# Kernel optimization log

Hardware: AMD Instinct MI355X
Metric: run time of the kernel (lower is better)

## Reference

```python
import jax, jax.numpy as jnp
import numpy as np

B, NZ, L = 8, 16, 512
E, DM, NH, HD = 256, 512, 16, 32
FF, NL, E1D, PDIM, PMAX = 1024, 8, 32, 64, 24
EPS_LN = 1e-5
EPS_D = 1e-12


def _ln(x, g, b):
    m = jnp.mean(x, axis=-1, keepdims=True)
    v = jnp.mean((x - m) ** 2, axis=-1, keepdims=True)
    return (x - m) / jnp.sqrt(v + EPS_LN) * g + b


def setup_inputs() -> dict:
    key = jax.random.key(0)
    ks = iter(jax.random.split(key, 32))
    rn = lambda shape, fan: jax.random.normal(next(ks), shape, jnp.float32) / np.float32(np.sqrt(fan))
    inp = {
        "z": jax.random.normal(next(ks), (B, NZ, L), jnp.float32),
        "x": jax.random.uniform(next(ks), (B, 20, L), jnp.float32),
        # embeddings
        "pos_table": rn((2 * PMAX + 1, PDIM), 1.0),
        "aa_table": rn((20, E1D), 1.0),
        # embed_x: Linear(nz,E), relu, Linear(E,E)
        "ex_w1": rn((NZ, E), NZ), "ex_b1": jnp.zeros((E,), jnp.float32),
        "ex_w2": rn((E, E), E), "ex_b2": jnp.zeros((E,), jnp.float32),
        # per-layer stacked params
        "Wq": rn((NL, E, DM), E), "Wk": rn((NL, E, DM), E), "Wv": rn((NL, E, DM), E),
        "Wo": rn((NL, DM, E), DM), "bo": jnp.zeros((NL, E), jnp.float32),
        "W2d": rn((NL, PDIM, NH), PDIM), "b2d": jnp.zeros((NL, NH), jnp.float32),
        "W1": rn((NL, E + E1D, FF), E + E1D), "b1": jnp.zeros((NL, FF), jnp.float32),
        "W2": rn((NL, FF, E), FF), "b2": jnp.zeros((NL, E), jnp.float32),
        "g1": jnp.ones((NL, E), jnp.float32), "be1": jnp.zeros((NL, E), jnp.float32),
        "g2": jnp.ones((NL, E), jnp.float32), "be2": jnp.zeros((NL, E), jnp.float32),
        # mlp_3d: Linear(E,E), relu, Linear(E,3)
        "m3_w1": rn((E, E), E), "m3_b1": jnp.zeros((E,), jnp.float32),
        "m3_w2": rn((E, 3), E), "m3_b2": jnp.zeros((3,), jnp.float32),
    }
    return inp


def reference(z, x, pos_table, aa_table, ex_w1, ex_b1, ex_w2, ex_b2,
              Wq, Wk, Wv, Wo, bo, W2d, b2d, W1, b1, W2, b2,
              g1, be1, g2, be2, m3_w1, m3_b1, m3_w2, m3_b2):
    Bn, _, Ln = z.shape
    h = jnp.transpose(z, (0, 2, 1))  # (B, L, nz)
    # relative-position bins: argmin over integer bins == clip to [-PMAX, PMAX]
    rel = jnp.arange(Ln)[None, :] - jnp.arange(Ln)[:, None]
    bins = jnp.clip(rel, -PMAX, PMAX) + PMAX
    pe = pos_table[bins]  # (L, L, PDIM), batch-replicated
    e_aa = aa_table[jnp.argmax(x, axis=1)]  # (B, L, E1D)
    # embed_x MLP
    h = jax.nn.relu(h @ ex_w1 + ex_b1) @ ex_w2 + ex_b2  # (B, L, E)
    scale = np.float32(1.0 / np.sqrt(DM))  # dp_attn_norm='d_model'
    for i in range(NL):
        q = (h @ Wq[i]).reshape(Bn, Ln, NH, HD) * scale
        k = (h @ Wk[i]).reshape(Bn, Ln, NH, HD)
        v = (h @ Wv[i]).reshape(Bn, Ln, NH, HD)
        # learned pairwise bias: mlp_2d then transpose(1,3).transpose(2,3) -> bias[h,i,j] = out[i,j,h]
        bias = jnp.einsum('lmp,ph->hlm', pe, W2d[i]) + b2d[i][:, None, None]
        scores = jnp.einsum('blhd,bmhd->bhlm', q, k) + bias[None]
        attn = jax.nn.softmax(scores, axis=-1)
        o = jnp.einsum('bhlm,bmhd->blhd', attn, v).reshape(Bn, Ln, DM)
        h = _ln(h + (o @ Wo[i] + bo[i]), g1[i], be1[i])
        um = jnp.concatenate([h, e_aa], axis=-1)  # (B, L, E+E1D)
        s2 = jax.nn.relu(um @ W1[i] + b1[i]) @ W2[i] + b2[i]
        h = _ln(h + s2, g2[i], be2[i])
    r = jax.nn.relu(h @ m3_w1 + m3_b1) @ m3_w2 + m3_b2  # (B, L, 3)
    # distance map (get_coords=False path)
    d = jnp.sqrt(jnp.sum((r[:, None, :, :] - r[:, :, None, :]) ** 2, axis=-1) + EPS_D)
    return d  # (B, L, L)
```

## Files before the change

kernel.cpp:

```cpp
#include <hip/hip_runtime.h>
#include <math.h>

constexpr int Bn = 8, NZ = 16, Ln = 512;
constexpr int E = 256, DM = 512, NH = 16, HD = 32;
constexpr int FF = 1024, NL = 8, E1D = 32, PDIM = 64, PMAX = 24;
constexpr int ROWS = Bn * Ln;
constexpr float QSCALE = 0.04419417382415922f;

typedef __attribute__((ext_vector_type(8))) short bf16x8;
typedef __attribute__((ext_vector_type(4))) float floatx4;

__device__ inline unsigned short f2b(float f) {
  union { float f; unsigned u; } v; v.f = f;
  unsigned r = (v.u + 0x7FFF + ((v.u >> 16) & 1)) >> 16;
  return (unsigned short)r;
}
__device__ inline float b2f(unsigned short u) {
  union { unsigned u; float f; } v; v.u = ((unsigned)u) << 16; return v.f;
}

__device__ inline void gll16(const void* g, void* l) {
  __builtin_amdgcn_global_load_lds(
      (const __attribute__((address_space(1))) void*)g,
      (__attribute__((address_space(3))) void*)l, 16, 0, 0);
}

__global__ __launch_bounds__(256) void transpose_qkv(
    const float* __restrict__ Wq, const float* __restrict__ Wk,
    const float* __restrict__ Wv, unsigned short* __restrict__ qkvT)
{
  __shared__ float t[32][33];
  int zb = blockIdx.z;
  int which = zb / NL, l = zb % NL;
  const float* s = (which == 0 ? Wq : which == 1 ? Wk : Wv) + (size_t)l * E * DM;
  unsigned short* d = qkvT + (size_t)l * 3 * DM * E + (size_t)which * DM * E;
  int c0 = blockIdx.x * 32, r0 = blockIdx.y * 32;
  int tx = threadIdx.x & 31, ty = threadIdx.x >> 5;
  #pragma unroll
  for (int i = 0; i < 4; ++i)
    t[ty + i * 8][tx] = s[(size_t)(r0 + ty + i * 8) * DM + c0 + tx];
  __syncthreads();
  #pragma unroll
  for (int i = 0; i < 4; ++i)
    d[(size_t)(c0 + ty + i * 8) * E + r0 + tx] = f2b(t[tx][ty + i * 8]);
}

__global__ __launch_bounds__(256) void transpose_bf16(
    const float* __restrict__ src, unsigned short* __restrict__ dst,
    int R, int C, size_t sls, size_t dls)
{
  __shared__ float t[32][33];
  int l = blockIdx.z;
  int c0 = blockIdx.x * 32, r0 = blockIdx.y * 32;
  int tx = threadIdx.x & 31, ty = threadIdx.x >> 5;
  const float* s = src + (size_t)l * sls;
  unsigned short* d = dst + (size_t)l * dls;
  #pragma unroll
  for (int i = 0; i < 4; ++i)
    t[ty + i * 8][tx] = s[(size_t)(r0 + ty + i * 8) * C + c0 + tx];
  __syncthreads();
  #pragma unroll
  for (int i = 0; i < 4; ++i)
    d[(size_t)(c0 + ty + i * 8) * R + r0 + tx] = f2b(t[tx][ty + i * 8]);
}

__global__ __launch_bounds__(256) void embed1_kernel(
    const float* __restrict__ z, const float* __restrict__ x,
    const float* __restrict__ aa,
    const float* __restrict__ w1, const float* __restrict__ b1,
    float* __restrict__ t0, unsigned short* __restrict__ umb)
{
  int row = blockIdx.x;
  int b = row >> 9, l = row & (Ln - 1);
  int t = threadIdx.x;
  __shared__ float zs[NZ];
  __shared__ int am_s;
  if (t < NZ) zs[t] = z[((size_t)b * NZ + t) * Ln + l];
  if (t == 0) {
    const float* xp = x + (size_t)b * 20 * Ln + l;
    int am = 0; float bv = xp[0];
    for (int c = 1; c < 20; ++c) { float vv = xp[(size_t)c * Ln]; if (vv > bv) { bv = vv; am = c; } }
    am_s = am;
  }
  __syncthreads();
  float a1 = b1[t];
  #pragma unroll
  for (int nz = 0; nz < NZ; ++nz) a1 += zs[nz] * w1[nz * E + t];
  t0[(size_t)row * E + t] = fmaxf(a1, 0.f);
  if (t < E1D) umb[(size_t)row * (E + E1D) + E + t] = f2b(aa[am_s * E1D + t]);
}

__global__ __launch_bounds__(256) void bias_kernel(
    const float* __restrict__ pos, const float* __restrict__ W2d,
    const float* __restrict__ b2d, float* __restrict__ bias49)
{
  int layer = blockIdx.x;
  for (int idx = threadIdx.x; idx < NH * 49; idx += 256) {
    int hh = idx / 49, bin = idx % 49;
    float acc = b2d[layer * NH + hh];
    for (int p = 0; p < PDIM; ++p)
      acc += pos[bin * PDIM + p] * W2d[((size_t)layer * PDIM + p) * NH + hh];
    bias49[(size_t)layer * NH * 49 + hh * 49 + bin] = acc;
  }
}

template<int BM, int BN, int BK, bool BIAS, bool RELU, bool OUTBF16, bool QKV>
__global__ __launch_bounds__(256) void gemm_mfma(
    const unsigned short* __restrict__ A, const unsigned short* __restrict__ Bt,
    const float* __restrict__ bias,
    float* __restrict__ Cf, unsigned short* __restrict__ Cb, int N, int K)
{
  constexpr int MT = BM / 32, NT = BN / 32;
  __shared__ __align__(16) unsigned short As[BM][BK];
  __shared__ __align__(16) unsigned short Bs[BN][BK];
  const int tid = threadIdx.x;
  const int wave = tid >> 6, ln = tid & 63;
  const int quad = ln >> 4, l16 = ln & 15;
  const int wm = wave >> 1, wn = wave & 1;
  const int m0 = blockIdx.y * BM, n0 = blockIdx.x * BN;

  floatx4 acc[MT][NT] = {};

  if constexpr (BK == 32) {
    const int lrow = ln >> 2, chunk = ln & 3;
    const int schunk = chunk ^ ((lrow >> 1) & 3);
    const unsigned short* aSrc = A + (size_t)(m0 + wave * 16 + lrow) * K + schunk * 8;
    const unsigned short* bSrc = Bt + (size_t)(n0 + wave * 16 + lrow) * K + schunk * 8;
    const int rkey = (l16 >> 1) & 3;

    for (int kb = 0; kb < K; kb += 32) {
      __syncthreads();
      #pragma unroll
      for (int it = 0; it < BM / 64; ++it)
        gll16(aSrc + (size_t)it * 64 * K + kb, &As[it * 64 + wave * 16][0]);
      #pragma unroll
      for (int it = 0; it < BN / 64; ++it)
        gll16(bSrc + (size_t)it * 64 * K + kb, &Bs[it * 64 + wave * 16][0]);
      __syncthreads();
      bf16x8 af[MT], bfr[NT];
      #pragma unroll
      for (int i = 0; i < MT; ++i)
        af[i] = *(const bf16x8*)&As[wm * (BM / 2) + i * 16 + l16][(quad ^ rkey) * 8];
      #pragma unroll
      for (int j = 0; j < NT; ++j)
        bfr[j] = *(const bf16x8*)&Bs[wn * (BN / 2) + j * 16 + l16][(quad ^ rkey) * 8];
      #pragma unroll
      for (int i = 0; i < MT; ++i)
        #pragma unroll
        for (int j = 0; j < NT; ++j)
          acc[i][j] = __builtin_amdgcn_mfma_f32_16x16x32_bf16(af[i], bfr[j], acc[i][j], 0, 0, 0);
    }
  } else {
    const int lrow = ln >> 4, chunk = ln & 15;
    const int key = wave * 4 + lrow;
    const int schunk = chunk ^ key;
    const unsigned short* aSrc = A + (size_t)(m0 + key) * K + schunk * 8;
    const unsigned short* bSrc = Bt + (size_t)(n0 + key) * K + schunk * 8;

    for (int kb = 0; kb < K; kb += 128) {
      __syncthreads();
      #pragma unroll
      for (int it = 0; it < BM / 16; ++it)
        gll16(aSrc + (size_t)(it * 16) * K + kb, &As[it * 16 + wave * 4][0]);
      #pragma unroll
      for (int it = 0; it < BN / 16; ++it)
        gll16(bSrc + (size_t)(it * 16) * K + kb, &Bs[it * 16 + wave * 4][0]);
      __syncthreads();
      #pragma unroll
      for (int kc = 0; kc < 4; ++kc) {
        bf16x8 af[MT], bfr[NT];
        #pragma unroll
        for (int i = 0; i < MT; ++i)
          af[i] = *(const bf16x8*)&As[wm * (BM / 2) + i * 16 + l16][(((kc * 4 + quad) ^ l16) * 8)];
        #pragma unroll
        for (int j = 0; j < NT; ++j)
          bfr[j] = *(const bf16x8*)&Bs[wn * (BN / 2) + j * 16 + l16][(((kc * 4 + quad) ^ l16) * 8)];
        #pragma unroll
        for (int i = 0; i < MT; ++i)
          #pragma unroll
          for (int j = 0; j < NT; ++j)
            acc[i][j] = __builtin_amdgcn_mfma_f32_16x16x32_bf16(af[i], bfr[j], acc[i][j], 0, 0, 0);
      }
    }
  }

  #pragma unroll
  for (int i = 0; i < MT; ++i)
    #pragma unroll
    for (int j = 0; j < NT; ++j) {
      int col = n0 + wn * (BN / 2) + j * 16 + l16;
      float bv = BIAS ? bias[col] : 0.f;
      float sc = QKV ? (col < 512 ? QSCALE : 1.f) : 1.f;
      #pragma unroll
      for (int r = 0; r < 4; ++r) {
        int rowg = m0 + wm * (BM / 2) + i * 16 + quad * 4 + r;
        float v = acc[i][j][r] * sc + bv;
        if (RELU) v = fmaxf(v, 0.f);
        if (OUTBF16) Cb[(size_t)rowg * N + col] = f2b(v);
        else Cf[(size_t)rowg * N + col] = v;
      }
    }
}

__global__ __launch_bounds__(256) void gemm_ln(
    const unsigned short* __restrict__ A, const unsigned short* __restrict__ Bt,
    const float* __restrict__ bias, float* __restrict__ h,
    const float* __restrict__ g, const float* __restrict__ be,
    unsigned short* __restrict__ outb, int bstride, int K)
{
  __shared__ __align__(16) unsigned short As[16][128];
  __shared__ __align__(16) unsigned short Bs[256][128];
  __shared__ __align__(16) float vtile[16][260];
  const int tid = threadIdx.x;
  const int w = tid >> 6, ln = tid & 63;
  const int quad = ln >> 4, l16 = ln & 15;
  const int m0 = blockIdx.x * 16;
  const int lrow = ln >> 4, chunk = ln & 15;
  const int key = w * 4 + lrow;
  const int schunk = chunk ^ key;
  const unsigned short* aSrc = A + (size_t)(m0 + key) * K + schunk * 8;
  const unsigned short* bSrc = Bt + (size_t)key * K + schunk * 8;

  floatx4 acc[4] = {};

  for (int kb = 0; kb < K; kb += 128) {
    __syncthreads();
    gll16(aSrc + kb, &As[w * 4][0]);
    #pragma unroll
    for (int it = 0; it < 16; ++it)
      gll16(bSrc + (size_t)(it * 16) * K + kb, &Bs[it * 16 + w * 4][0]);
    __syncthreads();
    #pragma unroll
    for (int kc = 0; kc < 4; ++kc) {
      bf16x8 af = *(const bf16x8*)&As[l16][(((kc * 4 + quad) ^ l16) * 8)];
      #pragma unroll
      for (int nt = 0; nt < 4; ++nt) {
        bf16x8 bf = *(const bf16x8*)&Bs[w * 64 + nt * 16 + l16][(((kc * 4 + quad) ^ l16) * 8)];
        acc[nt] = __builtin_amdgcn_mfma_f32_16x16x32_bf16(af, bf, acc[nt], 0, 0, 0);
      }
    }
  }

  #pragma unroll
  for (int nt = 0; nt < 4; ++nt) {
    int col = w * 64 + nt * 16 + l16;
    float bv = bias[col];
    #pragma unroll
    for (int r = 0; r < 4; ++r) {
      int row = quad * 4 + r;
      vtile[row][col] = acc[nt][r] + bv + h[(size_t)(m0 + row) * E + col];
    }
  }
  __syncthreads();

  const int c0 = ln * 4;
  #pragma unroll
  for (int rr = 0; rr < 4; ++rr) {
    const int lr = w * 4 + rr;
    float4 v = *(const float4*)&vtile[lr][c0];
    float s = v.x + v.y + v.z + v.w;
    float s2 = v.x * v.x + v.y * v.y + v.z * v.z + v.w * v.w;
    #pragma unroll
    for (int off = 1; off < 64; off <<= 1) {
      s += __shfl_xor(s, off, 64);
      s2 += __shfl_xor(s2, off, 64);
    }
    const float mean = s * (1.f / E);
    const float rstd = rsqrtf(s2 * (1.f / E) - mean * mean + 1e-5f);
    const float4 gv = *(const float4*)(g + c0);
    const float4 bv = *(const float4*)(be + c0);
    float4 y;
    y.x = (v.x - mean) * rstd * gv.x + bv.x;
    y.y = (v.y - mean) * rstd * gv.y + bv.y;
    y.z = (v.z - mean) * rstd * gv.z + bv.z;
    y.w = (v.w - mean) * rstd * gv.w + bv.w;
    const size_t row = (size_t)(m0 + lr);
    *(float4*)(h + row * E + c0) = y;
    ushort4 yb;
    yb.x = f2b(y.x); yb.y = f2b(y.y); yb.z = f2b(y.z); yb.w = f2b(y.w);
    *(ushort4*)(outb + row * (size_t)bstride + c0) = yb;
  }
}

__global__ __launch_bounds__(256) void attn_kernel(
    const unsigned short* __restrict__ qkv, const float* __restrict__ bias49,
    unsigned short* __restrict__ o)
{
  const int i0 = blockIdx.x * 64;
  const int bh = blockIdx.y;
  const int b = bh >> 4, hh = bh & 15;
  const int tid = threadIdx.x;
  const int wave = tid >> 6, ln = tid & 63;
  const int quad = ln >> 4, l16 = ln & 15;

  __shared__ __align__(16) unsigned short Kt[64][40];
  __shared__ __align__(16) unsigned short Vt[32][72];
  __shared__ __align__(16) unsigned short Pw[4][2][16][72];
  __shared__ float bsh[49];

  if (tid < 49) bsh[tid] = bias49[hh * 49 + tid];

  const unsigned short* qkvb = qkv + (size_t)b * Ln * 1536;

  const int qrow = i0 + wave * 16 + l16;
  const bf16x8 qf = *(const bf16x8*)(qkvb + (size_t)qrow * 1536 + hh * 32 + quad * 8);

  float m[4], l[4];
  #pragma unroll
  for (int r = 0; r < 4; ++r) { m[r] = -1e30f; l[r] = 0.f; }
  floatx4 acc_o[2] = {};

  const int krow = tid >> 2, kch = (tid & 3) * 8;
  const int vkey = tid & 63, vch = (tid >> 6) * 8;

  for (int jt = 0; jt < 8; ++jt) {
    const int j0 = jt * 64;
    __syncthreads();
    *(float4*)&Kt[krow][kch] =
        *(const float4*)(qkvb + (size_t)(j0 + krow) * 1536 + 512 + hh * 32 + kch);
    bf16x8 vv = *(const bf16x8*)(qkvb + (size_t)(j0 + vkey) * 1536 + 1024 + hh * 32 + vch);
    #pragma unroll
    for (int i = 0; i < 8; ++i) Vt[vch + i][vkey] = (unsigned short)vv[i];
    __syncthreads();

    floatx4 s4[4];
    #pragma unroll
    for (int t = 0; t < 4; ++t) {
      bf16x8 kf = *(const bf16x8*)&Kt[16 * t + l16][quad * 8];
      s4[t] = __builtin_amdgcn_mfma_f32_16x16x32_bf16(qf, kf, (floatx4){0.f, 0.f, 0.f, 0.f}, 0, 0, 0);
    }
    const int relmin = j0 - (i0 + 63), relmax = j0 + 63 - i0;
    if (relmin >= PMAX) {
      float bc = bsh[48];
      #pragma unroll
      for (int t = 0; t < 4; ++t)
        #pragma unroll
        for (int r = 0; r < 4; ++r) s4[t][r] += bc;
    } else if (relmax <= -PMAX) {
      float bc = bsh[0];
      #pragma unroll
      for (int t = 0; t < 4; ++t)
        #pragma unroll
        for (int r = 0; r < 4; ++r) s4[t][r] += bc;
    } else {
      const int base_rel = (j0 + l16) - (i0 + wave * 16 + quad * 4);
      #pragma unroll
      for (int t = 0; t < 4; ++t)
        #pragma unroll
        for (int r = 0; r < 4; ++r) {
          int rel = base_rel + 16 * t - r;
          rel = rel < -PMAX ? -PMAX : (rel > PMAX ? PMAX : rel);
          s4[t][r] += bsh[rel + PMAX];
        }
    }

    float mloc[4], alpha[4], psum[4];
    #pragma unroll
    for (int r = 0; r < 4; ++r) {
      mloc[r] = fmaxf(fmaxf(s4[0][r], s4[1][r]), fmaxf(s4[2][r], s4[3][r]));
      #pragma unroll
      for (int off = 1; off < 16; off <<= 1)
        mloc[r] = fmaxf(mloc[r], __shfl_xor(mloc[r], off, 64));
      float mnew = fmaxf(m[r], mloc[r]);
      alpha[r] = __expf(m[r] - mnew);
      m[r] = mnew;
      psum[r] = 0.f;
    }
    #pragma unroll
    for (int t = 0; t < 4; ++t)
      #pragma unroll
      for (int r = 0; r < 4; ++r) {
        float p = __expf(s4[t][r] - m[r]);
        s4[t][r] = p;
        psum[r] += p;
      }
    #pragma unroll
    for (int r = 0; r < 4; ++r) {
      #pragma unroll
      for (int off = 1; off < 16; off <<= 1)
        psum[r] += __shfl_xor(psum[r], off, 64);
      l[r] = l[r] * alpha[r] + psum[r];
      acc_o[0][r] *= alpha[r];
      acc_o[1][r] *= alpha[r];
    }

    #pragma unroll
    for (int t = 0; t < 4; ++t)
      #pragma unroll
      for (int r = 0; r < 4; ++r) {
        float p = s4[t][r];
        unsigned short hi = f2b(p);
        unsigned short lo = f2b(p - b2f(hi));
        Pw[wave][0][quad * 4 + r][16 * t + l16] = hi;
        Pw[wave][1][quad * 4 + r][16 * t + l16] = lo;
      }

    #pragma unroll
    for (int kh = 0; kh < 2; ++kh) {
      bf16x8 phi = *(const bf16x8*)&Pw[wave][0][l16][kh * 32 + quad * 8];
      bf16x8 plo = *(const bf16x8*)&Pw[wave][1][l16][kh * 32 + quad * 8];
      #pragma unroll
      for (int nt = 0; nt < 2; ++nt) {
        bf16x8 vf = *(const bf16x8*)&Vt[nt * 16 + l16][kh * 32 + quad * 8];
        acc_o[nt] = __builtin_amdgcn_mfma_f32_16x16x32_bf16(phi, vf, acc_o[nt], 0, 0, 0);
        acc_o[nt] = __builtin_amdgcn_mfma_f32_16x16x32_bf16(plo, vf, acc_o[nt], 0, 0, 0);
      }
    }
  }

  #pragma unroll
  for (int r = 0; r < 4; ++r) {
    float inv = 1.f / l[r];
    size_t rowg = (size_t)b * Ln + i0 + wave * 16 + quad * 4 + r;
    #pragma unroll
    for (int nt = 0; nt < 2; ++nt)
      o[rowg * 512 + hh * 32 + nt * 16 + l16] = f2b(acc_o[nt][r] * inv);
  }
}

template<bool RELU, bool BIAS, bool MIRROR>
__global__ __launch_bounds__(256) void gemm64f(
    const float* __restrict__ A, const float* __restrict__ B,
    const float* __restrict__ bias, float* __restrict__ C,
    unsigned short* __restrict__ mir, int N, int K)
{
  __shared__ __align__(16) float As[16][64];
  __shared__ __align__(16) float Bss[16][68];
  const int tid = threadIdx.x;
  const int tx = tid & 15, ty = tid >> 4;
  const int m0 = blockIdx.y * 64, n0 = blockIdx.x * 64;
  const int arow = tid >> 2, acol = (tid & 3) * 4;
  const int brow = tid >> 6, bcol = tid & 63;
  float acc[4][4] = {};
  for (int kb = 0; kb < K; kb += 16) {
    __syncthreads();
    float4 av = *(const float4*)(A + (size_t)(m0 + arow) * K + kb + acol);
    As[acol + 0][arow] = av.x; As[acol + 1][arow] = av.y;
    As[acol + 2][arow] = av.z; As[acol + 3][arow] = av.w;
    #pragma unroll
    for (int kk = 0; kk < 4; ++kk)
      Bss[brow + kk * 4][bcol] = B[(size_t)(kb + brow + kk * 4) * N + n0 + bcol];
    __syncthreads();
    #pragma unroll
    for (int k = 0; k < 16; ++k) {
      float4 a = *(const float4*)&As[k][4 * ty];
      float4 b = *(const float4*)&Bss[k][4 * tx];
      float av4[4] = {a.x, a.y, a.z, a.w};
      float bv4[4] = {b.x, b.y, b.z, b.w};
      #pragma unroll
      for (int ii = 0; ii < 4; ++ii)
        #pragma unroll
        for (int jj = 0; jj < 4; ++jj)
          acc[ii][jj] += av4[ii] * bv4[jj];
    }
  }
  #pragma unroll
  for (int ii = 0; ii < 4; ++ii) {
    size_t row = (size_t)m0 + 4 * ty + ii;
    int col = n0 + 4 * tx;
    float4 vv;
    vv.x = acc[ii][0]; vv.y = acc[ii][1]; vv.z = acc[ii][2]; vv.w = acc[ii][3];
    if (BIAS) {
      float4 bb = *(const float4*)(bias + col);
      vv.x += bb.x; vv.y += bb.y; vv.z += bb.z; vv.w += bb.w;
    }
    if (RELU) {
      vv.x = fmaxf(vv.x, 0.f); vv.y = fmaxf(vv.y, 0.f);
      vv.z = fmaxf(vv.z, 0.f); vv.w = fmaxf(vv.w, 0.f);
    }
    *(float4*)(C + row * N + col) = vv;
    if (MIRROR) {
      ushort4 mv;
      mv.x = f2b(vv.x); mv.y = f2b(vv.y); mv.z = f2b(vv.z); mv.w = f2b(vv.w);
      *(ushort4*)(mir + row * N + col) = mv;
    }
  }
}

__global__ __launch_bounds__(256) void final_r_kernel(
    const float* __restrict__ t1, const float* __restrict__ w2,
    const float* __restrict__ b2, float* __restrict__ r)
{
  int row = blockIdx.x, t = threadIdx.x;
  float xv = t1[(size_t)row * E + t];
  float p0 = xv * w2[t * 3 + 0];
  float p1 = xv * w2[t * 3 + 1];
  float p2 = xv * w2[t * 3 + 2];
  #pragma unroll
  for (int off = 32; off > 0; off >>= 1) {
    p0 += __shfl_down(p0, off, 64);
    p1 += __shfl_down(p1, off, 64);
    p2 += __shfl_down(p2, off, 64);
  }
  __shared__ float red[4][3];
  if ((t & 63) == 0) { int w = t >> 6; red[w][0] = p0; red[w][1] = p1; red[w][2] = p2; }
  __syncthreads();
  if (t < 3)
    r[(size_t)row * 3 + t] = red[0][t] + red[1][t] + red[2][t] + red[3][t] + b2[t];
}

__global__ __launch_bounds__(512) void dist_kernel(
    const float* __restrict__ r, float* __restrict__ out)
{
  int bi = blockIdx.x;
  int j = threadIdx.x;
  int b = bi >> 9;
  float x0 = r[(size_t)bi * 3 + 0];
  float y0 = r[(size_t)bi * 3 + 1];
  float z0 = r[(size_t)bi * 3 + 2];
  const float* rj = r + ((size_t)b * Ln + j) * 3;
  float dx = rj[0] - x0, dy = rj[1] - y0, dz = rj[2] - z0;
  out[(size_t)bi * Ln + j] = sqrtf(dx * dx + dy * dy + dz * dz + 1e-12f);
}

extern "C" void kernel_launch(void* const* d_in, const int* in_sizes, int n_in,
                              void* d_out, int out_size, void* d_ws, size_t ws_size,
                              hipStream_t stream)
{
  const float* z     = (const float*)d_in[0];
  const float* x     = (const float*)d_in[1];
  const float* pos   = (const float*)d_in[2];
  const float* aa    = (const float*)d_in[3];
  const float* ex_w1 = (const float*)d_in[4];
  const float* ex_b1 = (const float*)d_in[5];
  const float* ex_w2 = (const float*)d_in[6];
  const float* ex_b2 = (const float*)d_in[7];
  const float* Wq    = (const float*)d_in[8];
  const float* Wk    = (const float*)d_in[9];
  const float* Wv    = (const float*)d_in[10];
  const float* Wo    = (const float*)d_in[11];
  const float* bo    = (const float*)d_in[12];
  const float* W2d   = (const float*)d_in[13];
  const float* b2d   = (const float*)d_in[14];
  const float* W1    = (const float*)d_in[15];
  const float* b1    = (const float*)d_in[16];
  const float* W2    = (const float*)d_in[17];
  const float* b2    = (const float*)d_in[18];
  const float* g1    = (const float*)d_in[19];
  const float* be1   = (const float*)d_in[20];
  const float* g2    = (const float*)d_in[21];
  const float* be2   = (const float*)d_in[22];
  const float* m3w1  = (const float*)d_in[23];
  const float* m3b1  = (const float*)d_in[24];
  const float* m3w2  = (const float*)d_in[25];
  const float* m3b2  = (const float*)d_in[26];

  float* ws     = (float*)d_ws;
  float* h      = ws;
  float* t0     = h + (size_t)ROWS * E;
  float* r      = t0 + (size_t)ROWS * E;
  float* bias49 = r + (size_t)ROWS * 3;
  unsigned short* us = (unsigned short*)(bias49 + NL * NH * 49);
  unsigned short* hb   = us;
  unsigned short* umb  = hb  + (size_t)ROWS * E;
  unsigned short* qkvb = umb + (size_t)ROWS * (E + E1D);
  unsigned short* ob   = qkvb + (size_t)ROWS * 3 * DM;
  unsigned short* t1b  = ob  + (size_t)ROWS * DM;
  unsigned short* qkvT = t1b + (size_t)ROWS * FF;
  unsigned short* WoT  = qkvT + (size_t)NL * 3 * DM * E;
  unsigned short* W1T  = WoT  + (size_t)NL * E * DM;
  unsigned short* W2T  = W1T  + (size_t)NL * FF * (E+E1D);
  float* t1f = (float*)t1b;

  transpose_qkv<<<dim3(DM/32, E/32, 3*NL), 256, 0, stream>>>(Wq, Wk, Wv, qkvT);
  transpose_bf16<<<dim3(E/32, DM/32, NL), 256, 0, stream>>>(
      Wo, WoT, DM, E, (size_t)DM * E, (size_t)DM * E);
  transpose_bf16<<<dim3(FF/32, (E+E1D)/32, NL), 256, 0, stream>>>(
      W1, W1T, E + E1D, FF, (size_t)(E+E1D) * FF, (size_t)(E+E1D) * FF);
  transpose_bf16<<<dim3(E/32, FF/32, NL), 256, 0, stream>>>(
      W2, W2T, FF, E, (size_t)FF * E, (size_t)FF * E);

  embed1_kernel<<<ROWS, 256, 0, stream>>>(z, x, aa, ex_w1, ex_b1, t0, umb);
  gemm64f<false,true,true><<<dim3(E/64, ROWS/64), 256, 0, stream>>>(
      t0, ex_w2, ex_b2, h, hb, E, E);
  bias_kernel<<<NL, 256, 0, stream>>>(pos, W2d, b2d, bias49);

  for (int i = 0; i < NL; ++i) {
    gemm_mfma<64,128,128,false,false,true,true><<<dim3(12, 64), 256, 0, stream>>>(
        hb, qkvT + (size_t)i * 3 * DM * E, nullptr, nullptr, qkvb, 3 * DM, E);
    attn_kernel<<<dim3(Ln/64, Bn*NH), 256, 0, stream>>>(
        qkvb, bias49 + (size_t)i * NH * 49, ob);
    gemm_ln<<<ROWS/16, 256, 0, stream>>>(
        ob, WoT + (size_t)i * DM * E, bo + (size_t)i * E, h,
        g1 + (size_t)i * E, be1 + (size_t)i * E, umb, E + E1D, DM);
    gemm_mfma<64,64,32,true,true,true,false><<<dim3(FF/64, ROWS/64), 256, 0, stream>>>(
        umb, W1T + (size_t)i * FF * (E+E1D), b1 + (size_t)i * FF, nullptr, t1b, FF, E + E1D);
    gemm_ln<<<ROWS/16, 256, 0, stream>>>(
        t1b, W2T + (size_t)i * E * FF, b2 + (size_t)i * E, h,
        g2 + (size_t)i * E, be2 + (size_t)i * E, hb, E, FF);
  }

  gemm64f<true,true,false><<<dim3(E/64, ROWS/64), 256, 0, stream>>>(
      h, m3w1, m3b1, t1f, nullptr, E, E);
  final_r_kernel<<<ROWS, 256, 0, stream>>>(t1f, m3w2, m3b2, r);
  dist_kernel<<<ROWS, 512, 0, stream>>>(r, (float*)d_out);
}
```

Before: 813.6 us.

## Double-buffer K/V tiles with register prefetch and process 128 queries per block

```diff
diff --git a/kernel.cpp b/kernel.cpp
--- a/kernel.cpp
+++ b/kernel.cpp
@@ -286,15 +286,15 @@
     const unsigned short* __restrict__ qkv, const float* __restrict__ bias49,
     unsigned short* __restrict__ o)
 {
-  const int i0 = blockIdx.x * 64;
+  const int i0 = blockIdx.x * 128;
   const int bh = blockIdx.y;
   const int b = bh >> 4, hh = bh & 15;
   const int tid = threadIdx.x;
   const int wave = tid >> 6, ln = tid & 63;
   const int quad = ln >> 4, l16 = ln & 15;
 
-  __shared__ __align__(16) unsigned short Kt[64][40];
-  __shared__ __align__(16) unsigned short Vt[32][72];
+  __shared__ __align__(16) unsigned short Kt[2][64][40];
+  __shared__ __align__(16) unsigned short Vt[2][32][72];
   __shared__ __align__(16) unsigned short Pw[4][2][16][72];
   __shared__ float bsh[49];
 
@@ -302,120 +302,140 @@
 
   const unsigned short* qkvb = qkv + (size_t)b * Ln * 1536;
 
-  const int qrow = i0 + wave * 16 + l16;
-  const bf16x8 qf = *(const bf16x8*)(qkvb + (size_t)qrow * 1536 + hh * 32 + quad * 8);
-
-  float m[4], l[4];
-  #pragma unroll
-  for (int r = 0; r < 4; ++r) { m[r] = -1e30f; l[r] = 0.f; }
-  floatx4 acc_o[2] = {};
+  bf16x8 qf[2];
+  #pragma unroll
+  for (int u = 0; u < 2; ++u) {
+    const int qrow = i0 + wave * 32 + u * 16 + l16;
+    qf[u] = *(const bf16x8*)(qkvb + (size_t)qrow * 1536 + hh * 32 + quad * 8);
+  }
+
+  float m[2][4], l[2][4];
+  #pragma unroll
+  for (int u = 0; u < 2; ++u)
+    #pragma unroll
+    for (int r = 0; r < 4; ++r) { m[u][r] = -1e30f; l[u][r] = 0.f; }
+  floatx4 acc_o[2][2] = {};
 
   const int krow = tid >> 2, kch = (tid & 3) * 8;
   const int vkey = tid & 63, vch = (tid >> 6) * 8;
+  const unsigned short* kp = qkvb + (size_t)krow * 1536 + 512 + hh * 32 + kch;
+  const unsigned short* vp = qkvb + (size_t)vkey * 1536 + 1024 + hh * 32 + vch;
+
+  float4 kreg = *(const float4*)kp;
+  bf16x8 vreg = *(const bf16x8*)vp;
 
   for (int jt = 0; jt < 8; ++jt) {
     const int j0 = jt * 64;
+    const int cur = jt & 1;
+    *(float4*)&Kt[cur][krow][kch] = kreg;
+    #pragma unroll
+    for (int i = 0; i < 8; ++i) Vt[cur][vch + i][vkey] = (unsigned short)vreg[i];
     __syncthreads();
-    *(float4*)&Kt[krow][kch] =
-        *(const float4*)(qkvb + (size_t)(j0 + krow) * 1536 + 512 + hh * 32 + kch);
-    bf16x8 vv = *(const bf16x8*)(qkvb + (size_t)(j0 + vkey) * 1536 + 1024 + hh * 32 + vch);
-    #pragma unroll
-    for (int i = 0; i < 8; ++i) Vt[vch + i][vkey] = (unsigned short)vv[i];
-    __syncthreads();
-
-    floatx4 s4[4];
-    #pragma unroll
-    for (int t = 0; t < 4; ++t) {
-      bf16x8 kf = *(const bf16x8*)&Kt[16 * t + l16][quad * 8];
-      s4[t] = __builtin_amdgcn_mfma_f32_16x16x32_bf16(qf, kf, (floatx4){0.f, 0.f, 0.f, 0.f}, 0, 0, 0);
-    }
-    const int relmin = j0 - (i0 + 63), relmax = j0 + 63 - i0;
-    if (relmin >= PMAX) {
-      float bc = bsh[48];
+    if (jt < 7) {
+      kreg = *(const float4*)(kp + (size_t)(j0 + 64) * 1536);
+      vreg = *(const bf16x8*)(vp + (size_t)(j0 + 64) * 1536);
+    }
+
+    #pragma unroll
+    for (int u = 0; u < 2; ++u) {
+      const int qbase = i0 + wave * 32 + u * 16;
+
+      floatx4 s4[4];
+      #pragma unroll
+      for (int t = 0; t < 4; ++t) {
+        bf16x8 kf = *(const bf16x8*)&Kt[cur][16 * t + l16][quad * 8];
+        s4[t] = __builtin_amdgcn_mfma_f32_16x16x32_bf16(qf[u], kf, (floatx4){0.f, 0.f, 0.f, 0.f}, 0, 0, 0);
+      }
+      const int relmin = j0 - (qbase + 15), relmax = j0 + 63 - qbase;
+      if (relmin >= PMAX) {
+        float bc = bsh[48];
+        #pragma unroll
+        for (int t = 0; t < 4; ++t)
+          #pragma unroll
+          for (int r = 0; r < 4; ++r) s4[t][r] += bc;
+      } else if (relmax <= -PMAX) {
+        float bc = bsh[0];
+        #pragma unroll
+        for (int t = 0; t < 4; ++t)
+          #pragma unroll
+          for (int r = 0; r < 4; ++r) s4[t][r] += bc;
+      } else {
+        const int base_rel = (j0 + l16) - (qbase + quad * 4);
+        #pragma unroll
+        for (int t = 0; t < 4; ++t)
+          #pragma unroll
+          for (int r = 0; r < 4; ++r) {
+            int rel = base_rel + 16 * t - r;
+            rel = rel < -PMAX ? -PMAX : (rel > PMAX ? PMAX : rel);
+            s4[t][r] += bsh[rel + PMAX];
+          }
+      }
+
+      float mloc[4], alpha[4], psum[4];
+      #pragma unroll
+      for (int r = 0; r < 4; ++r) {
+        mloc[r] = fmaxf(fmaxf(s4[0][r], s4[1][r]), fmaxf(s4[2][r], s4[3][r]));
+        #pragma unroll
+        for (int off = 1; off < 16; off <<= 1)
+          mloc[r] = fmaxf(mloc[r], __shfl_xor(mloc[r], off, 64));
+        float mnew = fmaxf(m[u][r], mloc[r]);
+        alpha[r] = __expf(m[u][r] - mnew);
+        m[u][r] = mnew;
+        psum[r] = 0.f;
+      }
       #pragma unroll
       for (int t = 0; t < 4; ++t)
         #pragma unroll
-        for (int r = 0; r < 4; ++r) s4[t][r] += bc;
-    } else if (relmax <= -PMAX) {
-      float bc = bsh[0];
+        for (int r = 0; r < 4; ++r) {
+          float p = __expf(s4[t][r] - m[u][r]);
+          s4[t][r] = p;
+          psum[r] += p;
+        }
+      #pragma unroll
+      for (int r = 0; r < 4; ++r) {
+        #pragma unroll
+        for (int off = 1; off < 16; off <<= 1)
+          psum[r] += __shfl_xor(psum[r], off, 64);
+        l[u][r] = l[u][r] * alpha[r] + psum[r];
+        acc_o[u][0][r] *= alpha[r];
+        acc_o[u][1][r] *= alpha[r];
+      }
+
       #pragma unroll
       for (int t = 0; t < 4; ++t)
         #pragma unroll
-        for (int r = 0; r < 4; ++r) s4[t][r] += bc;
-    } else {
-      const int base_rel = (j0 + l16) - (i0 + wave * 16 + quad * 4);
-      #pragma unroll
-      for (int t = 0; t < 4; ++t)
-        #pragma unroll
         for (int r = 0; r < 4; ++r) {
-          int rel = base_rel + 16 * t - r;
-          rel = rel < -PMAX ? -PMAX : (rel > PMAX ? PMAX : rel);
-          s4[t][r] += bsh[rel + PMAX];
+          float p = s4[t][r];
+          unsigned short hi = f2b(p);
+          unsigned short lo = f2b(p - b2f(hi));
+          Pw[wave][0][quad * 4 + r][16 * t + l16] = hi;
+          Pw[wave][1][quad * 4 + r][16 * t + l16] = lo;
         }
-    }
-
-    float mloc[4], alpha[4], psum[4];
+
+      #pragma unroll
+      for (int kh = 0; kh < 2; ++kh) {
+        bf16x8 phi = *(const bf16x8*)&Pw[wave][0][l16][kh * 32 + quad * 8];
+        bf16x8 plo = *(const bf16x8*)&Pw[wave][1][l16][kh * 32 + quad * 8];
+        #pragma unroll
+        for (int nt = 0; nt < 2; ++nt) {
+          bf16x8 vf = *(const bf16x8*)&Vt[cur][nt * 16 + l16][kh * 32 + quad * 8];
+          acc_o[u][nt] = __builtin_amdgcn_mfma_f32_16x16x32_bf16(phi, vf, acc_o[u][nt], 0, 0, 0);
+          acc_o[u][nt] = __builtin_amdgcn_mfma_f32_16x16x32_bf16(plo, vf, acc_o[u][nt], 0, 0, 0);
+        }
+      }
+    }
+  }
+
+  #pragma unroll
+  for (int u = 0; u < 2; ++u)
     #pragma unroll
     for (int r = 0; r < 4; ++r) {
-      mloc[r] = fmaxf(fmaxf(s4[0][r], s4[1][r]), fmaxf(s4[2][r], s4[3][r]));
-      #pragma unroll
-      for (int off = 1; off < 16; off <<= 1)
-        mloc[r] = fmaxf(mloc[r], __shfl_xor(mloc[r], off, 64));
-      float mnew = fmaxf(m[r], mloc[r]);
-      alpha[r] = __expf(m[r] - mnew);
-      m[r] = mnew;
-      psum[r] = 0.f;
-    }
-    #pragma unroll
-    for (int t = 0; t < 4; ++t)
-      #pragma unroll
-      for (int r = 0; r < 4; ++r) {
-        float p = __expf(s4[t][r] - m[r]);
-        s4[t][r] = p;
-        psum[r] += p;
-      }
-    #pragma unroll
-    for (int r = 0; r < 4; ++r) {
-      #pragma unroll
-      for (int off = 1; off < 16; off <<= 1)
-        psum[r] += __shfl_xor(psum[r], off, 64);
-      l[r] = l[r] * alpha[r] + psum[r];
-      acc_o[0][r] *= alpha[r];
-      acc_o[1][r] *= alpha[r];
-    }
-
-    #pragma unroll
-    for (int t = 0; t < 4; ++t)
-      #pragma unroll
-      for (int r = 0; r < 4; ++r) {
-        float p = s4[t][r];
-        unsigned short hi = f2b(p);
-        unsigned short lo = f2b(p - b2f(hi));
-        Pw[wave][0][quad * 4 + r][16 * t + l16] = hi;
-        Pw[wave][1][quad * 4 + r][16 * t + l16] = lo;
-      }
-
-    #pragma unroll
-    for (int kh = 0; kh < 2; ++kh) {
-      bf16x8 phi = *(const bf16x8*)&Pw[wave][0][l16][kh * 32 + quad * 8];
-      bf16x8 plo = *(const bf16x8*)&Pw[wave][1][l16][kh * 32 + quad * 8];
-      #pragma unroll
-      for (int nt = 0; nt < 2; ++nt) {
-        bf16x8 vf = *(const bf16x8*)&Vt[nt * 16 + l16][kh * 32 + quad * 8];
-        acc_o[nt] = __builtin_amdgcn_mfma_f32_16x16x32_bf16(phi, vf, acc_o[nt], 0, 0, 0);
-        acc_o[nt] = __builtin_amdgcn_mfma_f32_16x16x32_bf16(plo, vf, acc_o[nt], 0, 0, 0);
-      }
-    }
-  }
-
-  #pragma unroll
-  for (int r = 0; r < 4; ++r) {
-    float inv = 1.f / l[r];
-    size_t rowg = (size_t)b * Ln + i0 + wave * 16 + quad * 4 + r;
-    #pragma unroll
-    for (int nt = 0; nt < 2; ++nt)
-      o[rowg * 512 + hh * 32 + nt * 16 + l16] = f2b(acc_o[nt][r] * inv);
-  }
+      float inv = 1.f / l[u][r];
+      size_t rowg = (size_t)b * Ln + i0 + wave * 32 + u * 16 + quad * 4 + r;
+      #pragma unroll
+      for (int nt = 0; nt < 2; ++nt)
+        o[rowg * 512 + hh * 32 + nt * 16 + l16] = f2b(acc_o[u][nt][r] * inv);
+    }
 }
 
 template<bool RELU, bool BIAS, bool MIRROR>
@@ -578,7 +598,7 @@
   for (int i = 0; i < NL; ++i) {
     gemm_mfma<64,128,128,false,false,true,true><<<dim3(12, 64), 256, 0, stream>>>(
         hb, qkvT + (size_t)i * 3 * DM * E, nullptr, nullptr, qkvb, 3 * DM, E);
-    attn_kernel<<<dim3(Ln/64, Bn*NH), 256, 0, stream>>>(
+    attn_kernel<<<dim3(Ln/128, Bn*NH), 256, 0, stream>>>(
         qkvb, bias49 + (size_t)i * NH * 49, ob);
     gemm_ln<<<ROWS/16, 256, 0, stream>>>(
         ob, WoT + (size_t)i * DM * E, bo + (size_t)i * E, h,
```

Measured after the change: 862.1 us. +6.0%, slower.
